# Optimization experiments

Hardware: AMD Instinct MI355X
Metric: run time of the kernel (lower is better)

Reference implementation:

```python
import jax, jax.numpy as jnp
import numpy as np

N_NODES = 100000
N_EDGES = 3200000
N_GRAPHS = 256


def setup_inputs() -> dict:
    key = jax.random.key(0)
    ks = jax.random.split(key, 8)
    x = jax.random.normal(ks[0], (N_NODES, 13), dtype=jnp.float32)
    edge_index = jax.random.randint(ks[1], (2, N_EDGES), 0, N_NODES, dtype=jnp.int64)
    batch = jnp.sort(jax.random.randint(ks[2], (N_NODES,), 0, N_GRAPHS, dtype=jnp.int64))
    W1 = jax.random.normal(ks[3], (13, 64), dtype=jnp.float32) * 0.1
    b1 = jnp.zeros((64,), dtype=jnp.float32)
    W2 = jax.random.normal(ks[4], (64, 64), dtype=jnp.float32) * 0.1
    b2 = jnp.zeros((64,), dtype=jnp.float32)
    W3 = jax.random.normal(ks[5], (64, 32), dtype=jnp.float32) * 0.1
    b3 = jnp.zeros((32,), dtype=jnp.float32)
    return {"x": x, "edge_index": edge_index, "batch": batch,
            "W1": W1, "b1": b1, "W2": W2, "b2": b2, "W3": W3, "b3": b3}


def _gcn_norm(edge_index, num_nodes):
    # PyG GCNConv default: add self-loops, symmetric D^-1/2 (A+I) D^-1/2 normalization.
    loops = jnp.arange(num_nodes, dtype=edge_index.dtype)
    src = jnp.concatenate([edge_index[0], loops])
    dst = jnp.concatenate([edge_index[1], loops])
    ones = jnp.ones(src.shape[0], dtype=jnp.float32)
    deg = jax.ops.segment_sum(ones, dst, num_segments=num_nodes)
    dinv = jnp.where(deg > 0, jax.lax.rsqrt(deg), 0.0)
    norm = dinv[src] * dinv[dst]  # [E+N]
    return src, dst, norm


def _gcn_conv(h, W, b, src, dst, norm, num_nodes):
    h = h @ W                                   # [N, out]
    msg = h[src] * norm[:, None]                # gather + scale, [E+N, out]
    out = jax.ops.segment_sum(msg, dst, num_segments=num_nodes)  # scatter-add
    return out + b


def reference(x, edge_index, batch, W1, b1, W2, b2, W3, b3):
    n = x.shape[0]
    src, dst, norm = _gcn_norm(edge_index, n)
    h = jax.nn.relu(_gcn_conv(x, W1, b1, src, dst, norm, n))
    h = jax.nn.relu(_gcn_conv(h, W2, b2, src, dst, norm, n))
    h = _gcn_conv(h, W3, b3, src, dst, norm, n)
    # global_mean_pool over graphs
    sums = jax.ops.segment_sum(h, batch, num_segments=N_GRAPHS)
    counts = jax.ops.segment_sum(jnp.ones((n,), jnp.float32), batch, num_segments=N_GRAPHS)
    return sums / jnp.maximum(counts, 1.0)[:, None]
```

## Files before the change

### kernel.cpp

```cpp
#include <hip/hip_runtime.h>
#include <hip/hip_fp16.h>

constexpr int NN = 100000;
constexpr int NE = 3200000;
constexpr int NG = 256;
constexpr int NCB = 196;
constexpr int TILE = 4096;
constexpr int EPT = TILE / 256;
constexpr int CAP = 17408;

__global__ void k_zero_i(int* __restrict__ p, int n) {
  int i = blockIdx.x * blockDim.x + threadIdx.x;
  if (i < n) p[i] = 0;
}

__global__ void k_cscan(const int* __restrict__ gcursor, int* __restrict__ cbase) {
  __shared__ int s[256];
  const int t = threadIdx.x;
  s[t] = (t < NCB) ? gcursor[t] : 0;
  __syncthreads();
  for (int o = 1; o < 256; o <<= 1) {
    int v = s[t];
    int u = (t >= o) ? s[t - o] : 0;
    __syncthreads();
    s[t] = v + u;
    __syncthreads();
  }
  if (t < NCB) cbase[t] = (t == 0) ? 0 : s[t - 1];
  if (t == 0) cbase[NCB] = NE;
}

__global__ void k_msplit(const int* __restrict__ src, const int* __restrict__ dst,
                         int* __restrict__ gcursor, int* __restrict__ pairs, int E) {
  constexpr int NT = 256;
  __shared__ int hist[NCB], lbase[NCB], lcur[NCB], gwrite[NCB];
  __shared__ int staged[TILE];
  __shared__ unsigned char sbid[TILE];
  __shared__ int stot;
  const int tid = threadIdx.x;
  const int e0 = blockIdx.x * TILE;
  for (int i = tid; i < NCB; i += NT) { hist[i] = 0; lcur[i] = 0; }
  __syncthreads();
  int ls[EPT], ld[EPT];
#pragma unroll
  for (int i = 0; i < EPT; ++i) {
    int e = e0 + i * NT + tid;
    if (e < E) {
      ls[i] = src[e];
      ld[i] = dst[e];
      atomicAdd(&hist[ld[i] >> 9], 1);
    } else {
      ld[i] = -1;
    }
  }
  __syncthreads();
  if (tid == 0) {
    int run = 0;
    for (int c = 0; c < NCB; ++c) { lbase[c] = run; run += hist[c]; }
    stot = run;
  }
  __syncthreads();
  for (int c = tid; c < NCB; c += NT) {
    int cnt = hist[c];
    if (cnt > 0) {
      int g = atomicAdd(&gcursor[c], cnt);
      gwrite[c] = c * CAP + g;
    }
  }
  __syncthreads();
#pragma unroll
  for (int i = 0; i < EPT; ++i) {
    if (ld[i] >= 0) {
      int c = ld[i] >> 9;
      int pos = lbase[c] + atomicAdd(&lcur[c], 1);
      staged[pos] = ls[i] | ((ld[i] & 511) << 17);
      sbid[pos] = (unsigned char)c;
    }
  }
  __syncthreads();
  const int total = stot;
  for (int i = tid; i < total; i += NT) {
    int c = sbid[i];
    pairs[gwrite[c] + (i - lbase[c])] = staged[i];
  }
}

__global__ void k_brow(const int* __restrict__ pairs, const int* __restrict__ cbase,
                       int* __restrict__ rowstart, float* __restrict__ dinv,
                       int* __restrict__ csr_src) {
  __shared__ int deg[512], pre[512], cur[512];
  __shared__ int s[256];
  const int cb = blockIdx.x;
  const int n0 = cb << 9;
  const int tid = threadIdx.x;
  const int e0 = cbase[cb];
  const int cnt = cbase[cb + 1] - e0;
  const int p0 = cb * CAP;
  for (int i = tid; i < 512; i += 256) { deg[i] = 0; cur[i] = 0; }
  __syncthreads();
  for (int e = tid; e < cnt; e += 256) atomicAdd(&deg[pairs[p0 + e] >> 17], 1);
  __syncthreads();
  int d0 = deg[2 * tid], d1 = deg[2 * tid + 1];
  s[tid] = d0 + d1;
  __syncthreads();
  for (int o = 1; o < 256; o <<= 1) {
    int v = s[tid];
    int u = (tid >= o) ? s[tid - o] : 0;
    __syncthreads();
    s[tid] = v + u;
    __syncthreads();
  }
  int p2 = (tid == 0) ? 0 : s[tid - 1];
  pre[2 * tid] = p2;
  pre[2 * tid + 1] = p2 + d0;
  __syncthreads();
  for (int i = tid; i < 512; i += 256) {
    int n = n0 + i;
    if (n < NN) {
      rowstart[n] = e0 + pre[i];
      dinv[n] = rsqrtf((float)(deg[i] + 1));
    }
  }
  if (cb == NCB - 1 && tid == 0) rowstart[NN] = NE;
  for (int e = tid; e < cnt; e += 256) {
    int w = pairs[p0 + e];
    int dl = w >> 17;
    int p = e0 + pre[dl] + atomicAdd(&cur[dl], 1);
    csr_src[p] = w & 0x1FFFF;
  }
}

__global__ void k_xs(const float* __restrict__ x, const float* __restrict__ dinv,
                     __half* __restrict__ xs) {
  int i = blockIdx.x * blockDim.x + threadIdx.x;
  if (i < NN * 16) {
    int v = i >> 4, f = i & 15;
    float val = (f < 13) ? x[v * 13 + f] * dinv[v] : 0.0f;
    xs[i] = __float2half_rn(val);
  }
}

__global__ void k_gather16(const __half* __restrict__ xs, const int* __restrict__ rowstart,
                           const int* __restrict__ csr_src, const float* __restrict__ dinv,
                           float* __restrict__ agg) {
  __shared__ int lidx[4][64];
  const int wv = threadIdx.x >> 6;
  const int node = (blockIdx.x * blockDim.x + threadIdx.x) >> 6;
  const int lane = threadIdx.x & 63;
  const int fp = lane & 7;
  const int es = lane >> 3;
  const __half2* x2 = (const __half2*)xs;
  const int r0 = rowstart[node], r1 = rowstart[node + 1];
  float ax = 0.0f, ay = 0.0f;
  if (es == 0) {
    float2 sf = __half22float2(x2[node * 8 + fp]);
    ax = sf.x; ay = sf.y;
  }
  for (int base = r0; base < r1; base += 64) {
    const int nc = min(64, r1 - base);
    lidx[wv][lane] = (base + lane < r1) ? csr_src[base + lane] : 0;
    int i = es;
    for (; i + 24 < nc; i += 32) {
      int s0 = lidx[wv][i], s1 = lidx[wv][i + 8], s2 = lidx[wv][i + 16], s3 = lidx[wv][i + 24];
      float2 v0 = __half22float2(x2[s0 * 8 + fp]);
      float2 v1 = __half22float2(x2[s1 * 8 + fp]);
      float2 v2 = __half22float2(x2[s2 * 8 + fp]);
      float2 v3 = __half22float2(x2[s3 * 8 + fp]);
      ax += (v0.x + v1.x) + (v2.x + v3.x);
      ay += (v0.y + v1.y) + (v2.y + v3.y);
    }
    for (; i < nc; i += 8) {
      int s = lidx[wv][i];
      float2 v = __half22float2(x2[s * 8 + fp]);
      ax += v.x; ay += v.y;
    }
  }
  ax += __shfl_xor(ax, 32); ay += __shfl_xor(ay, 32);
  ax += __shfl_xor(ax, 16); ay += __shfl_xor(ay, 16);
  ax += __shfl_xor(ax, 8);  ay += __shfl_xor(ay, 8);
  if (lane < 8) {
    const float di = dinv[node];
    ((float2*)agg)[node * 8 + lane] = make_float2(ax * di, ay * di);
  }
}

__global__ void k_mmfused(const float* __restrict__ agg, const float* __restrict__ W1,
                          const float* __restrict__ b1, const float* __restrict__ W2,
                          const float* __restrict__ dinv, __half* __restrict__ t2, int n) {
  __shared__ float Ws1[13 * 64];
  __shared__ float Bs1[64];
  __shared__ float Ws2[64 * 64];
  __shared__ float Hs[4][16];
  __shared__ float H1[4][64];
  const int tid = threadIdx.x;
  for (int i = tid; i < 13 * 64; i += 256) Ws1[i] = W1[i];
  if (tid < 64) Bs1[tid] = b1[tid];
  for (int i = tid; i < 64 * 64; i += 256) Ws2[i] = W2[i];
  const int row0 = blockIdx.x * 4;
  for (int i = tid; i < 4 * 16; i += 256) {
    int rr = i >> 4, kk = i & 15;
    int gr = row0 + rr;
    Hs[rr][kk] = (gr < n) ? agg[gr * 16 + kk] : 0.0f;
  }
  __syncthreads();
  const int r = tid >> 6, c = tid & 63;
  float acc = Bs1[c];
#pragma unroll
  for (int k = 0; k < 13; ++k) acc += Hs[r][k] * Ws1[k * 64 + c];
  H1[r][c] = fmaxf(acc, 0.0f);
  __syncthreads();
  const int row = row0 + r;
  if (row < n) {
    float a2 = 0.0f;
#pragma unroll
    for (int k = 0; k < 64; ++k) a2 += H1[r][k] * Ws2[k * 64 + c];
    t2[row * 64 + c] = __float2half_rn(a2 * dinv[row]);
  }
}

__global__ void __launch_bounds__(256) k_gather64m(
    const __half* __restrict__ t, const int* __restrict__ rowstart,
    const int* __restrict__ csr_src, const float* __restrict__ dinv,
    const float* __restrict__ b2, const float* __restrict__ W3,
    __half* __restrict__ t3) {
  __shared__ float W3s[64 * 32];
  __shared__ float h2s[4][64];
  __shared__ int lidx[4][64];
  const int tid = threadIdx.x;
  for (int i = tid; i < 64 * 32; i += 256) W3s[i] = W3[i];
  __syncthreads();
  const int w = tid >> 6;
  const int lane = tid & 63;
  const int node = blockIdx.x * 4 + w;
  const int fp = lane & 31;
  const int es = lane >> 5;
  const __half2* t2 = (const __half2*)t;
  const int r0 = rowstart[node], r1 = rowstart[node + 1];
  float ax = 0.0f, ay = 0.0f;
  if (es == 0) {
    float2 sf = __half22float2(t2[node * 32 + fp]);
    ax = sf.x; ay = sf.y;
  }
  for (int base = r0; base < r1; base += 64) {
    const int nc = min(64, r1 - base);
    lidx[w][lane] = (base + lane < r1) ? csr_src[base + lane] : 0;
    int i = es;
    for (; i + 14 < nc; i += 16) {
      int s0 = lidx[w][i],      s1 = lidx[w][i + 2],  s2 = lidx[w][i + 4],  s3 = lidx[w][i + 6];
      int s4 = lidx[w][i + 8],  s5 = lidx[w][i + 10], s6 = lidx[w][i + 12], s7 = lidx[w][i + 14];
      float2 v0 = __half22float2(t2[s0 * 32 + fp]);
      float2 v1 = __half22float2(t2[s1 * 32 + fp]);
      float2 v2 = __half22float2(t2[s2 * 32 + fp]);
      float2 v3 = __half22float2(t2[s3 * 32 + fp]);
      float2 v4 = __half22float2(t2[s4 * 32 + fp]);
      float2 v5 = __half22float2(t2[s5 * 32 + fp]);
      float2 v6 = __half22float2(t2[s6 * 32 + fp]);
      float2 v7 = __half22float2(t2[s7 * 32 + fp]);
      ax += ((v0.x + v1.x) + (v2.x + v3.x)) + ((v4.x + v5.x) + (v6.x + v7.x));
      ay += ((v0.y + v1.y) + (v2.y + v3.y)) + ((v4.y + v5.y) + (v6.y + v7.y));
    }
    for (; i < nc; i += 2) {
      int s = lidx[w][i];
      float2 v = __half22float2(t2[s * 32 + fp]);
      ax += v.x; ay += v.y;
    }
  }
  ax += __shfl_xor(ax, 32); ay += __shfl_xor(ay, 32);
  const float di = dinv[node];
  if (es == 0) {
    float2 bb = ((const float2*)b2)[fp];
    h2s[w][2 * fp]     = fmaxf(ax * di + bb.x, 0.0f);
    h2s[w][2 * fp + 1] = fmaxf(ay * di + bb.y, 0.0f);
  }
  const int j = lane & 31, kh = lane >> 5;
  float p = 0.0f;
#pragma unroll
  for (int k2 = 0; k2 < 32; ++k2) {
    int k = kh * 32 + k2;
    p += h2s[w][k] * W3s[k * 32 + j];
  }
  p += __shfl_xor(p, 32);
  if (lane < 32) t3[node * 32 + j] = __float2half_rn(p * di);
}

__global__ void k_gather32w(const __half* __restrict__ t, const int* __restrict__ rowstart,
                            const int* __restrict__ csr_src,
                            const float* __restrict__ dinv, const float* __restrict__ b,
                            __half* __restrict__ h3) {
  __shared__ int lidx[4][64];
  const int wv = threadIdx.x >> 6;
  const int node = (blockIdx.x * blockDim.x + threadIdx.x) >> 6;
  const int lane = threadIdx.x & 63;
  const int fp = lane & 15;
  const int es = lane >> 4;
  const __half2* t2 = (const __half2*)t;
  const int r0 = rowstart[node], r1 = rowstart[node + 1];
  float ax = 0.0f, ay = 0.0f;
  if (es == 0) {
    float2 sf = __half22float2(t2[node * 16 + fp]);
    ax = sf.x; ay = sf.y;
  }
  for (int base = r0; base < r1; base += 64) {
    const int nc = min(64, r1 - base);
    lidx[wv][lane] = (base + lane < r1) ? csr_src[base + lane] : 0;
    int i = es;
    for (; i + 28 < nc; i += 32) {
      int s0 = lidx[wv][i],      s1 = lidx[wv][i + 4],  s2 = lidx[wv][i + 8],  s3 = lidx[wv][i + 12];
      int s4 = lidx[wv][i + 16], s5 = lidx[wv][i + 20], s6 = lidx[wv][i + 24], s7 = lidx[wv][i + 28];
      float2 v0 = __half22float2(t2[s0 * 16 + fp]);
      float2 v1 = __half22float2(t2[s1 * 16 + fp]);
      float2 v2 = __half22float2(t2[s2 * 16 + fp]);
      float2 v3 = __half22float2(t2[s3 * 16 + fp]);
      float2 v4 = __half22float2(t2[s4 * 16 + fp]);
      float2 v5 = __half22float2(t2[s5 * 16 + fp]);
      float2 v6 = __half22float2(t2[s6 * 16 + fp]);
      float2 v7 = __half22float2(t2[s7 * 16 + fp]);
      ax += ((v0.x + v1.x) + (v2.x + v3.x)) + ((v4.x + v5.x) + (v6.x + v7.x));
      ay += ((v0.y + v1.y) + (v2.y + v3.y)) + ((v4.y + v5.y) + (v6.y + v7.y));
    }
    for (; i < nc; i += 4) {
      int s = lidx[wv][i];
      float2 v = __half22float2(t2[s * 16 + fp]);
      ax += v.x; ay += v.y;
    }
  }
  ax += __shfl_xor(ax, 32); ay += __shfl_xor(ay, 32);
  ax += __shfl_xor(ax, 16); ay += __shfl_xor(ay, 16);
  if (lane < 16) {
    const float di = dinv[node];
    float2 bb = ((const float2*)b)[fp];
    ((__half2*)h3)[node * 16 + fp] = __floats2half2_rn(ax * di + bb.x, ay * di + bb.y);
  }
}

__global__ void k_pool(const __half* __restrict__ h3, const int* __restrict__ batch,
                       float* __restrict__ out) {
  const int g = blockIdx.x;
  int lo = 0, hi = NN;
  while (lo < hi) { int m = (lo + hi) >> 1; if (batch[m] < g) lo = m + 1; else hi = m; }
  const int a = lo;
  lo = 0; hi = NN;
  while (lo < hi) { int m = (lo + hi) >> 1; if (batch[m] < g + 1) lo = m + 1; else hi = m; }
  const int bEnd = lo;
  const int tid = threadIdx.x;
  const int nl = tid >> 4, f = tid & 15;
  const __half2* h2p = (const __half2*)h3;
  float ax = 0.0f, ay = 0.0f;
  for (int n = a + nl; n < bEnd; n += 16) {
    float2 v = __half22float2(h2p[n * 16 + f]);
    ax += v.x; ay += v.y;
  }
  __shared__ float redx[16][16], redy[16][16];
  redx[nl][f] = ax; redy[nl][f] = ay;
  __syncthreads();
  if (tid < 16) {
    float sx = 0.0f, sy = 0.0f;
#pragma unroll
    for (int i = 0; i < 16; ++i) { sx += redx[i][tid]; sy += redy[i][tid]; }
    float inv = 1.0f / fmaxf((float)(bEnd - a), 1.0f);
    ((float2*)out)[g * 16 + tid] = make_float2(sx * inv, sy * inv);
  }
}

extern "C" void kernel_launch(void* const* d_in, const int* in_sizes, int n_in,
                              void* d_out, int out_size, void* d_ws, size_t ws_size,
                              hipStream_t stream) {
  const float* x  = (const float*)d_in[0];
  const int*   ei = (const int*)d_in[1];
  const int* batch = (const int*)d_in[2];
  const float* W1 = (const float*)d_in[3];
  const float* b1 = (const float*)d_in[4];
  const float* W2 = (const float*)d_in[5];
  const float* b2 = (const float*)d_in[6];
  const float* W3 = (const float*)d_in[7];
  const float* b3 = (const float*)d_in[8];
  float* out = (float*)d_out;

  const int* src = ei;
  const int* dst = ei + NE;

  float* ws = (float*)d_ws;
  float* dinv     = ws;
  int*   gcursor  = (int*)(ws + 100352);
  int*   cbase    = (int*)(ws + 100608);
  int*   rowstart = (int*)(ws + 100944);
  int*   csr_src  = (int*)(ws + 201056);
  float* bufT     = ws + 3401056;
  float* bufH     = ws + 9801056;
  int*    pairs = (int*)bufT;
  __half* t2    = (__half*)bufT;
  __half* h3    = (__half*)(bufT + 1600000);
  __half* xs    = (__half*)bufH;
  float*  agg1  = bufH + 1600000;
  __half* t3    = (__half*)bufH;

  const int B = 256;
  auto cdiv = [](int a, int b) { return (a + b - 1) / b; };

  k_zero_i<<<1, B, 0, stream>>>(gcursor, NCB);
  k_msplit<<<cdiv(NE, TILE), B, 0, stream>>>(src, dst, gcursor, pairs, NE);
  k_cscan<<<1, 256, 0, stream>>>(gcursor, cbase);
  k_brow<<<NCB, B, 0, stream>>>(pairs, cbase, rowstart, dinv, csr_src);

  k_xs<<<cdiv(NN * 16, B), B, 0, stream>>>(x, dinv, xs);
  k_gather16<<<cdiv(NN * 64, B), B, 0, stream>>>(xs, rowstart, csr_src, dinv, agg1);
  k_mmfused<<<cdiv(NN, 4), B, 0, stream>>>(agg1, W1, b1, W2, dinv, t2, NN);

  k_gather64m<<<NN / 4, B, 0, stream>>>(t2, rowstart, csr_src, dinv, b2, W3, t3);

  k_gather32w<<<cdiv(NN * 64, B), B, 0, stream>>>(t3, rowstart, csr_src, dinv, b3, h3);
  k_pool<<<NG, B, 0, stream>>>(h3, batch, out);
}
```

Before: 333.4 us.

## Fuse layer-1 gather with MLP, fold column scan into k_brow, vectorize msplit loads

The layer-1 neighbor gather is merged with the W1/ReLU/W2 matmul kernel, so aggregated features stay in shared memory instead of round-tripping through a global buffer, and one launch is removed. The separate bucket-offset scan kernel is dropped; each k_brow block now recomputes the prefix sum of bucket counts itself. k_msplit loads src/dst as int4 vectors to cut load instructions. In exchange, each fused block reloads the full W1/W2 weights into shared memory for only four nodes, and every k_brow block repeats the small scan.

```diff
diff --git a/kernel.cpp b/kernel.cpp
--- a/kernel.cpp
+++ b/kernel.cpp
@@ -14,22 +14,6 @@
   if (i < n) p[i] = 0;
 }
 
-__global__ void k_cscan(const int* __restrict__ gcursor, int* __restrict__ cbase) {
-  __shared__ int s[256];
-  const int t = threadIdx.x;
-  s[t] = (t < NCB) ? gcursor[t] : 0;
-  __syncthreads();
-  for (int o = 1; o < 256; o <<= 1) {
-    int v = s[t];
-    int u = (t >= o) ? s[t - o] : 0;
-    __syncthreads();
-    s[t] = v + u;
-    __syncthreads();
-  }
-  if (t < NCB) cbase[t] = (t == 0) ? 0 : s[t - 1];
-  if (t == 0) cbase[NCB] = NE;
-}
-
 __global__ void k_msplit(const int* __restrict__ src, const int* __restrict__ dst,
                          int* __restrict__ gcursor, int* __restrict__ pairs, int E) {
   constexpr int NT = 256;
@@ -41,16 +25,19 @@
   const int e0 = blockIdx.x * TILE;
   for (int i = tid; i < NCB; i += NT) { hist[i] = 0; lcur[i] = 0; }
   __syncthreads();
-  int ls[EPT], ld[EPT];
-#pragma unroll
-  for (int i = 0; i < EPT; ++i) {
-    int e = e0 + i * NT + tid;
-    if (e < E) {
-      ls[i] = src[e];
-      ld[i] = dst[e];
-      atomicAdd(&hist[ld[i] >> 9], 1);
-    } else {
-      ld[i] = -1;
+  int4 ls[EPT / 4], ld[EPT / 4];
+  bool valid[EPT / 4];
+#pragma unroll
+  for (int j = 0; j < EPT / 4; ++j) {
+    int e = e0 + j * (NT * 4) + tid * 4;
+    valid[j] = (e < E);
+    if (valid[j]) {
+      ls[j] = *(const int4*)(src + e);
+      ld[j] = *(const int4*)(dst + e);
+      atomicAdd(&hist[ld[j].x >> 9], 1);
+      atomicAdd(&hist[ld[j].y >> 9], 1);
+      atomicAdd(&hist[ld[j].z >> 9], 1);
+      atomicAdd(&hist[ld[j].w >> 9], 1);
     }
   }
   __syncthreads();
@@ -69,12 +56,17 @@
   }
   __syncthreads();
 #pragma unroll
-  for (int i = 0; i < EPT; ++i) {
-    if (ld[i] >= 0) {
-      int c = ld[i] >> 9;
-      int pos = lbase[c] + atomicAdd(&lcur[c], 1);
-      staged[pos] = ls[i] | ((ld[i] & 511) << 17);
-      sbid[pos] = (unsigned char)c;
+  for (int j = 0; j < EPT / 4; ++j) {
+    if (valid[j]) {
+      int ss[4] = {ls[j].x, ls[j].y, ls[j].z, ls[j].w};
+      int dd[4] = {ld[j].x, ld[j].y, ld[j].z, ld[j].w};
+#pragma unroll
+      for (int q = 0; q < 4; ++q) {
+        int c = dd[q] >> 9;
+        int pos = lbase[c] + atomicAdd(&lcur[c], 1);
+        staged[pos] = ss[q] | ((dd[q] & 511) << 17);
+        sbid[pos] = (unsigned char)c;
+      }
     }
   }
   __syncthreads();
@@ -85,7 +77,7 @@
   }
 }
 
-__global__ void k_brow(const int* __restrict__ pairs, const int* __restrict__ cbase,
+__global__ void k_brow(const int* __restrict__ pairs, const int* __restrict__ gcursor,
                        int* __restrict__ rowstart, float* __restrict__ dinv,
                        int* __restrict__ csr_src) {
   __shared__ int deg[512], pre[512], cur[512];
@@ -93,9 +85,19 @@
   const int cb = blockIdx.x;
   const int n0 = cb << 9;
   const int tid = threadIdx.x;
-  const int e0 = cbase[cb];
-  const int cnt = cbase[cb + 1] - e0;
+  s[tid] = (tid < NCB) ? gcursor[tid] : 0;
+  __syncthreads();
+  for (int o = 1; o < 256; o <<= 1) {
+    int v = s[tid];
+    int u = (tid >= o) ? s[tid - o] : 0;
+    __syncthreads();
+    s[tid] = v + u;
+    __syncthreads();
+  }
+  const int e0 = (cb == 0) ? 0 : s[cb - 1];
+  const int cnt = gcursor[cb];
   const int p0 = cb * CAP;
+  __syncthreads();
   for (int i = tid; i < 512; i += 256) { deg[i] = 0; cur[i] = 0; }
   __syncthreads();
   for (int e = tid; e < cnt; e += 256) atomicAdd(&deg[pairs[p0 + e] >> 17], 1);
@@ -140,13 +142,25 @@
   }
 }
 
-__global__ void k_gather16(const __half* __restrict__ xs, const int* __restrict__ rowstart,
-                           const int* __restrict__ csr_src, const float* __restrict__ dinv,
-                           float* __restrict__ agg) {
+__global__ void __launch_bounds__(256) k_l1fused(
+    const __half* __restrict__ xs, const int* __restrict__ rowstart,
+    const int* __restrict__ csr_src, const float* __restrict__ dinv,
+    const float* __restrict__ W1, const float* __restrict__ b1,
+    const float* __restrict__ W2, __half* __restrict__ t2) {
+  __shared__ float W1s[13 * 64];
+  __shared__ float B1s[64];
+  __shared__ float W2s[64 * 64];
+  __shared__ float aggs[4][16];
+  __shared__ float h1s[4][64];
   __shared__ int lidx[4][64];
-  const int wv = threadIdx.x >> 6;
-  const int node = (blockIdx.x * blockDim.x + threadIdx.x) >> 6;
-  const int lane = threadIdx.x & 63;
+  const int tid = threadIdx.x;
+  for (int i = tid; i < 13 * 64; i += 256) W1s[i] = W1[i];
+  if (tid < 64) B1s[tid] = b1[tid];
+  for (int i = tid; i < 64 * 64; i += 256) W2s[i] = W2[i];
+  __syncthreads();
+  const int wv = tid >> 6;
+  const int lane = tid & 63;
+  const int node = blockIdx.x * 4 + wv;
   const int fp = lane & 7;
   const int es = lane >> 3;
   const __half2* x2 = (const __half2*)xs;
@@ -178,44 +192,19 @@
   ax += __shfl_xor(ax, 32); ay += __shfl_xor(ay, 32);
   ax += __shfl_xor(ax, 16); ay += __shfl_xor(ay, 16);
   ax += __shfl_xor(ax, 8);  ay += __shfl_xor(ay, 8);
+  const float di = dinv[node];
   if (lane < 8) {
-    const float di = dinv[node];
-    ((float2*)agg)[node * 8 + lane] = make_float2(ax * di, ay * di);
-  }
-}
-
-__global__ void k_mmfused(const float* __restrict__ agg, const float* __restrict__ W1,
-                          const float* __restrict__ b1, const float* __restrict__ W2,
-                          const float* __restrict__ dinv, __half* __restrict__ t2, int n) {
-  __shared__ float Ws1[13 * 64];
-  __shared__ float Bs1[64];
-  __shared__ float Ws2[64 * 64];
-  __shared__ float Hs[4][16];
-  __shared__ float H1[4][64];
-  const int tid = threadIdx.x;
-  for (int i = tid; i < 13 * 64; i += 256) Ws1[i] = W1[i];
-  if (tid < 64) Bs1[tid] = b1[tid];
-  for (int i = tid; i < 64 * 64; i += 256) Ws2[i] = W2[i];
-  const int row0 = blockIdx.x * 4;
-  for (int i = tid; i < 4 * 16; i += 256) {
-    int rr = i >> 4, kk = i & 15;
-    int gr = row0 + rr;
-    Hs[rr][kk] = (gr < n) ? agg[gr * 16 + kk] : 0.0f;
-  }
-  __syncthreads();
-  const int r = tid >> 6, c = tid & 63;
-  float acc = Bs1[c];
-#pragma unroll
-  for (int k = 0; k < 13; ++k) acc += Hs[r][k] * Ws1[k * 64 + c];
-  H1[r][c] = fmaxf(acc, 0.0f);
-  __syncthreads();
-  const int row = row0 + r;
-  if (row < n) {
-    float a2 = 0.0f;
-#pragma unroll
-    for (int k = 0; k < 64; ++k) a2 += H1[r][k] * Ws2[k * 64 + c];
-    t2[row * 64 + c] = __float2half_rn(a2 * dinv[row]);
-  }
+    aggs[wv][2 * fp]     = ax * di;
+    aggs[wv][2 * fp + 1] = ay * di;
+  }
+  float acc = B1s[lane];
+#pragma unroll
+  for (int k = 0; k < 13; ++k) acc += aggs[wv][k] * W1s[k * 64 + lane];
+  h1s[wv][lane] = fmaxf(acc, 0.0f);
+  float a2 = 0.0f;
+#pragma unroll
+  for (int k = 0; k < 64; ++k) a2 += h1s[wv][k] * W2s[k * 64 + lane];
+  t2[node * 64 + lane] = __float2half_rn(a2 * di);
 }
 
 __global__ void __launch_bounds__(256) k_gather64m(
@@ -382,7 +371,6 @@
   float* ws = (float*)d_ws;
   float* dinv     = ws;
   int*   gcursor  = (int*)(ws + 100352);
-  int*   cbase    = (int*)(ws + 100608);
   int*   rowstart = (int*)(ws + 100944);
   int*   csr_src  = (int*)(ws + 201056);
   float* bufT     = ws + 3401056;
@@ -391,7 +379,6 @@
   __half* t2    = (__half*)bufT;
   __half* h3    = (__half*)(bufT + 1600000);
   __half* xs    = (__half*)bufH;
-  float*  agg1  = bufH + 1600000;
   __half* t3    = (__half*)bufH;
 
   const int B = 256;
@@ -399,12 +386,10 @@
 
   k_zero_i<<<1, B, 0, stream>>>(gcursor, NCB);
   k_msplit<<<cdiv(NE, TILE), B, 0, stream>>>(src, dst, gcursor, pairs, NE);
-  k_cscan<<<1, 256, 0, stream>>>(gcursor, cbase);
-  k_brow<<<NCB, B, 0, stream>>>(pairs, cbase, rowstart, dinv, csr_src);
+  k_brow<<<NCB, B, 0, stream>>>(pairs, gcursor, rowstart, dinv, csr_src);
 
   k_xs<<<cdiv(NN * 16, B), B, 0, stream>>>(x, dinv, xs);
-  k_gather16<<<cdiv(NN * 64, B), B, 0, stream>>>(xs, rowstart, csr_src, dinv, agg1);
-  k_mmfused<<<cdiv(NN, 4), B, 0, stream>>>(agg1, W1, b1, W2, dinv, t2, NN);
+  k_l1fused<<<NN / 4, B, 0, stream>>>(xs, rowstart, csr_src, dinv, W1, b1, W2, t2);
 
   k_gather64m<<<NN / 4, B, 0, stream>>>(t2, rowstart, csr_src, dinv, b2, W3, t3);
 
```

Result: faster. 319.9 us (-4.0%).
